# Optimization experiments

Measured on AMD Instinct MI355X. Metric: run time of the kernel, lower is better.

## Reference

```python
import jax, jax.numpy as jnp
import numpy as np

T, B, D, H, OUT = 128, 256, 512, 768, 60


def setup_inputs() -> dict:
    key = jax.random.key(0)
    ks = jax.random.split(key, 8)
    def xavier(k, shape):
        fan_out, fan_in = shape
        limit = np.sqrt(6.0 / (fan_in + fan_out))
        return jax.random.uniform(k, shape, jnp.float32, -limit, limit)
    inp = {
        "input_sample": jax.random.normal(ks[0], (T, B, D), jnp.float32),
        # PyTorch LSTMCell params: weight_ih (4H, D), weight_hh (4H, H), biases (4H,)
        "W_ih": xavier(ks[1], (4 * H, D)),
        "W_hh": xavier(ks[2], (4 * H, H)),
        "b_ih": jax.random.uniform(ks[3], (4 * H,), jnp.float32, -1 / np.sqrt(H), 1 / np.sqrt(H)),
        "b_hh": jax.random.uniform(ks[4], (4 * H,), jnp.float32, -1 / np.sqrt(H), 1 / np.sqrt(H)),
        "W_fc": xavier(ks[5], (OUT, H)),
        "b_fc": jnp.zeros((OUT,), jnp.float32),
    }
    return inp


def _lstm_head(input_sample, W_ih, W_hh, b_ih, b_hh, W_fc, b_fc):
    B_ = input_sample.shape[1]
    H_ = W_hh.shape[1]
    # Precompute input projections for all time steps in one GEMM: (T, B, 4H)
    x_proj = jnp.einsum("tbd,gd->tbg", input_sample, W_ih) + b_ih + b_hh

    def step(carry, xp_t):
        h, c = carry
        gates = xp_t + h @ W_hh.T  # (B, 4H)
        i, f, g, o = jnp.split(gates, 4, axis=-1)  # PyTorch gate order: i, f, g, o
        i = jax.nn.sigmoid(i)
        f = jax.nn.sigmoid(f)
        g = jnp.tanh(g)
        o = jax.nn.sigmoid(o)
        c_new = f * c + i * g
        h_new = o * jnp.tanh(c_new)
        return (h_new, c_new), None

    h0 = jnp.zeros((B_, H_), input_sample.dtype)
    c0 = jnp.zeros((B_, H_), input_sample.dtype)
    (h_T, _), _ = jax.lax.scan(step, (h0, c0), x_proj)
    return h_T @ W_fc.T + b_fc  # (B, OUT)


def reference(input_sample, W_ih, W_hh, b_ih, b_hh, W_fc, b_fc):
    return _lstm_head(input_sample, W_ih, W_hh, b_ih, b_hh, W_fc, b_fc)
```

## Files before the change

kernel.cpp:

```cpp
#include <hip/hip_runtime.h>
#include <stdint.h>

#define T_ 128
#define B_ 256
#define D_ 512
#define H_ 768
#define NG 3072
#define OUT_ 60

using bf16x8 = __attribute__((ext_vector_type(8))) __bf16;
using f32x4  = __attribute__((ext_vector_type(4))) float;
using u32x4  = __attribute__((ext_vector_type(4))) unsigned int;

#define OFF_XB   ((size_t)0)
#define OFF_WI   (OFF_XB + (size_t)T_*B_*D_*2)
#define OFF_WHPK (OFF_WI + (size_t)NG*D_*2)
#define OFF_H    (OFF_WHPK + (size_t)NG*H_*2)
#define OFF_HT   (OFF_H + (size_t)2*B_*H_*2)
#define OFF_BAR  (OFF_HT + (size_t)B_*H_*4)
#define OFF_XP   (OFF_BAR + 65536)
#define OFF_END  (OFF_XP + (size_t)T_*B_*NG*2)

__device__ __forceinline__ unsigned short f2bf(float f) {
  union { float f; unsigned u; } v; v.f = f;
  unsigned r = (v.u + 0x7fffu + ((v.u >> 16) & 1u)) >> 16;
  return (unsigned short)r;
}
__device__ __forceinline__ float sigf(float x) {
  return __builtin_amdgcn_rcpf(1.0f + __expf(-x));
}
__device__ __forceinline__ float tanhf_(float x) {
  return 2.0f * __builtin_amdgcn_rcpf(1.0f + __expf(-2.0f * x)) - 1.0f;
}
__device__ __forceinline__ void gload16(const void* g, void* l) {
  __builtin_amdgcn_global_load_lds(
      (const __attribute__((address_space(1))) unsigned int*)g,
      (__attribute__((address_space(3))) unsigned int*)l, 16, 0, 0);
}
template<int OFF, bool SC1>
__device__ __forceinline__ u32x4 ld16(const void* p) {
  u32x4 r;
  if constexpr (SC1)
    asm volatile("global_load_dwordx4 %0, %1, off offset:%c2 sc0 sc1"
                 : "=v"(r) : "v"(p), "i"(OFF) : "memory");
  else
    asm volatile("global_load_dwordx4 %0, %1, off offset:%c2 sc0"
                 : "=v"(r) : "v"(p), "i"(OFF) : "memory");
  return r;
}
__device__ __forceinline__ unsigned ld4coh(const unsigned* p) {
  unsigned r;
  asm volatile("global_load_dword %0, %1, off sc0 sc1\n\ts_waitcnt vmcnt(0)"
               : "=v"(r) : "v"(p) : "memory");
  return r;
}
template<bool SC1>
__device__ __forceinline__ void st2(ushort* p, unsigned v) {
  if constexpr (SC1)
    asm volatile("global_store_short %0, %1, off sc0 sc1" :: "v"(p), "v"(v) : "memory");
  else
    asm volatile("global_store_short %0, %1, off sc0" :: "v"(p), "v"(v) : "memory");
}
__device__ __forceinline__ void st4coh(unsigned* p, unsigned v) {
  asm volatile("global_store_dword %0, %1, off sc0 sc1" :: "v"(p), "v"(v) : "memory");
}

__global__ void prep_kernel(const float* __restrict__ x,
                            const float* __restrict__ wihf,
                            const float* __restrict__ whhf,
                            uint8_t* __restrict__ ws) {
  ushort* xb = (ushort*)(ws + OFF_XB);
  ushort* wi = (ushort*)(ws + OFF_WI);
  ushort* whpk = (ushort*)(ws + OFF_WHPK);
  unsigned* bar = (unsigned*)(ws + OFF_BAR);
  const size_t tid = (size_t)blockIdx.x * blockDim.x + threadIdx.x;
  const size_t nth = (size_t)gridDim.x * blockDim.x;

  for (size_t i = tid; i < (size_t)T_*B_*D_/4; i += nth) {
    float4 v = ((const float4*)x)[i];
    ushort4 o; o.x=f2bf(v.x); o.y=f2bf(v.y); o.z=f2bf(v.z); o.w=f2bf(v.w);
    ((ushort4*)xb)[i] = o;
  }
  for (size_t i = tid; i < (size_t)NG*D_/4; i += nth) {
    float4 v = ((const float4*)wihf)[i];
    ushort4 o; o.x=f2bf(v.x); o.y=f2bf(v.y); o.z=f2bf(v.z); o.w=f2bf(v.w);
    ((ushort4*)wi)[i] = o;
  }
  for (size_t c = tid; c < (size_t)294912; c += nth) {
    const unsigned L = (unsigned)c & 63u;
    const unsigned r1 = (unsigned)(c >> 6);
    const unsigned nt = r1 % 6u, r2 = r1 / 6u;
    const unsigned kf = r2 % 24u, s = r2 / 24u;
    const unsigned i = nt*16u + (L & 15u);
    const unsigned G = (i & 3u)*768u + s*24u + (i >> 2);
    const unsigned k0 = kf*32u + (L >> 4)*8u;
    const float4 v0 = *(const float4*)(whhf + (size_t)G*768u + k0);
    const float4 v1 = *(const float4*)(whhf + (size_t)G*768u + k0 + 4);
    ushort4 o0, o1;
    o0.x=f2bf(v0.x); o0.y=f2bf(v0.y); o0.z=f2bf(v0.z); o0.w=f2bf(v0.w);
    o1.x=f2bf(v1.x); o1.y=f2bf(v1.y); o1.z=f2bf(v1.z); o1.w=f2bf(v1.w);
    *(ushort4*)(whpk + c*8)     = o0;
    *(ushort4*)(whpk + c*8 + 4) = o1;
  }
  for (size_t i = tid; i < 16384; i += nth) bar[i] = 0u;
}

__global__ __launch_bounds__(256) void xproj_kernel(uint8_t* __restrict__ ws) {
  const ushort* __restrict__ xb = (const ushort*)(ws + OFF_XB);
  const ushort* __restrict__ wi = (const ushort*)(ws + OFF_WI);
  ushort* __restrict__ xp = (ushort*)(ws + OFF_XP);

  __shared__ ushort smA[128*64];
  __shared__ ushort smB[128*64];

  const int tid = threadIdx.x;
  const int lane = tid & 63;
  const int w = tid >> 6;
  const int bn = blockIdx.x % 24;
  const int bm = blockIdx.x / 24;
  const int m0 = bm * 128, n0 = bn * 128;
  const int mi = (w >> 1) * 64, ni = (w & 1) * 64;

  f32x4 acc[4][4] = {};

  for (int k0 = 0; k0 < D_; k0 += 64) {
    __syncthreads();
    #pragma unroll
    for (int i = 0; i < 4; ++i) {
      const int ig = w*4 + i;
      const int o  = ig*1024 + lane*16;
      const int row = o >> 7;
      const int colB = o & 127;
      const int scol = colB ^ ((row & 7) << 4);
      gload16((const uint8_t*)xb + ((size_t)(m0+row)*D_ + k0)*2 + scol,
              (uint8_t*)smA + ig*1024);
      gload16((const uint8_t*)wi + ((size_t)(n0+row)*D_ + k0)*2 + scol,
              (uint8_t*)smB + ig*1024);
    }
    __syncthreads();
    #pragma unroll
    for (int kk = 0; kk < 2; ++kk) {
      const int colB = kk*64 + (lane >> 4)*16;
      bf16x8 a[4], b[4];
      #pragma unroll
      for (int mt = 0; mt < 4; ++mt) {
        const int row = mi + mt*16 + (lane & 15);
        a[mt] = *(const bf16x8*)((const uint8_t*)smA + row*128 + (colB ^ ((row & 7) << 4)));
      }
      #pragma unroll
      for (int nt = 0; nt < 4; ++nt) {
        const int row = ni + nt*16 + (lane & 15);
        b[nt] = *(const bf16x8*)((const uint8_t*)smB + row*128 + (colB ^ ((row & 7) << 4)));
      }
      #pragma unroll
      for (int mt = 0; mt < 4; ++mt)
        #pragma unroll
        for (int nt = 0; nt < 4; ++nt)
          acc[mt][nt] = __builtin_amdgcn_mfma_f32_16x16x32_bf16(a[mt], b[nt], acc[mt][nt], 0, 0, 0);
    }
  }
  #pragma unroll
  for (int mt = 0; mt < 4; ++mt)
    #pragma unroll
    for (int nt = 0; nt < 4; ++nt) {
      const int r0 = m0 + mi + mt*16 + (lane >> 4)*4;
      const int c  = n0 + ni + nt*16 + (lane & 15);
      #pragma unroll
      for (int r = 0; r < 4; ++r)
        xp[(size_t)(r0 + r)*NG + c] = f2bf(acc[mt][nt][r]);
    }
}

template<bool SC1>
__device__ __forceinline__ void run_loop(uint8_t* ws, const ushort* whh_lds, float* gbuf,
                                         const float* bih, const float* bhh,
                                         int tid, int g, int s) {
  const int lane = tid & 63, w = tid >> 6, wq = w & 1, wm = w >> 1;
  const int l15 = lane & 15, hi = lane >> 4;
  ushort* hb = (ushort*)(ws + OFF_H);
  const ushort* xp = (const ushort*)(ws + OFF_XP);
  float* hT = (float*)(ws + OFF_HT);
  unsigned* bar = (unsigned*)(ws + OFF_BAR);
  float* gw = gbuf + w*816;

  float bias[3][4];
  #pragma unroll
  for (int j = 0; j < 3; ++j) {
    const int col = s*24 + wq*12 + hi + 4*j;
    #pragma unroll
    for (int q = 0; q < 4; ++q) bias[j][q] = bih[q*H_ + col] + bhh[q*H_ + col];
  }
  const unsigned* fp = bar + (size_t)(g*32 + ((lane < 32) ? lane : 31)) * 16;

  const ushort* xpb = xp + (size_t)(g*32 + wm*16 + l15)*NG + s*24 + wq*12 + hi;
  ushort xq[12];
  {
    const ushort* p = xpb;
    #pragma unroll
    for (int q = 0; q < 4; ++q)
      #pragma unroll
      for (int j = 0; j < 3; ++j)
        xq[q*3+j] = p[q*768 + 4*j];
  }

  float cc[3] = {0.f, 0.f, 0.f};

  #pragma unroll 1
  for (int t = 0; t < T_; ++t) {
    f32x4 acc[3] = {};
    if (t > 0) {
      if (w == 0) {
        while (1) {
          const unsigned v = ld4coh(fp);
          if (__all((int)(v >= (unsigned)t))) break;
          __builtin_amdgcn_s_sleep(1);
        }
      }
      __syncthreads();
      const ushort* hr = hb + ((size_t)(t & 1)*8 + g)*((size_t)32*H_)
                         + (size_t)(wm*16 + l15)*H_ + hi*8;
      u32x4 ah[24];
      #define LH(i) ah[i] = ld16<(i)*64, SC1>(hr)
      LH(0); LH(1); LH(2); LH(3); LH(4); LH(5); LH(6); LH(7);
      LH(8); LH(9); LH(10); LH(11); LH(12); LH(13); LH(14); LH(15);
      LH(16); LH(17); LH(18); LH(19); LH(20); LH(21); LH(22); LH(23);
      #undef LH
      asm volatile("s_waitcnt vmcnt(0)" ::: "memory");
      __builtin_amdgcn_sched_barrier(0);
      #pragma unroll
      for (int kf = 0; kf < 24; ++kf) {
        const bf16x8 a = *(const bf16x8*)&ah[kf];
        #pragma unroll
        for (int n = 0; n < 3; ++n) {
          const bf16x8 b = *(const bf16x8*)(whh_lds + (size_t)((kf*6 + wq*3 + n)*64 + lane)*8);
          acc[n] = __builtin_amdgcn_mfma_f32_16x16x32_bf16(a, b, acc[n], 0, 0, 0);
        }
      }
    }
    #pragma unroll
    for (int n = 0; n < 3; ++n)
      #pragma unroll
      for (int r = 0; r < 4; ++r)
        gw[(n*16 + l15)*17 + hi*4 + r] = acc[n][r];
    float hv[3];
    #pragma unroll
    for (int j = 0; j < 3; ++j) {
      const int cl = hi + 4*j;
      float gq[4];
      #pragma unroll
      for (int q = 0; q < 4; ++q) {
        union { unsigned u; float f; } xv; xv.u = ((unsigned)xq[q*3 + j]) << 16;
        gq[q] = gw[(cl*4+q)*17 + l15] + xv.f + bias[j][q];
      }
      const float iv = sigf(gq[0]);
      const float fv = sigf(gq[1]);
      const float gv = tanhf_(gq[2]);
      const float ov = sigf(gq[3]);
      const float cn = fv*cc[j] + iv*gv;
      cc[j] = cn;
      hv[j] = ov * tanhf_(cn);
    }
    const int rowl = wm*16 + l15;
    if (t == T_-1) {
      #pragma unroll
      for (int j = 0; j < 3; ++j) {
        const int col = s*24 + wq*12 + hi + 4*j;
        hT[(size_t)(g*32 + rowl)*H_ + col] = hv[j];
      }
      break;
    }
    ushort* hn = hb + ((size_t)((t+1) & 1)*8 + g)*((size_t)32*H_);
    #pragma unroll
    for (int j = 0; j < 3; ++j) {
      const int col = s*24 + wq*12 + hi + 4*j;
      st2<SC1>(hn + (size_t)rowl*H_ + col, (unsigned)f2bf(hv[j]));
    }
    asm volatile("s_waitcnt vmcnt(0)" ::: "memory");
    __syncthreads();
    if (tid == 0) st4coh(bar + (size_t)(g*32 + s)*16, (unsigned)(t + 1));
    {
      const ushort* p = xpb + (size_t)(t + 1)*B_*NG;
      #pragma unroll
      for (int q = 0; q < 4; ++q)
        #pragma unroll
        for (int j = 0; j < 3; ++j)
          xq[q*3+j] = p[q*768 + 4*j];
    }
  }
}

__global__ __launch_bounds__(256, 1) void lstm_kernel(uint8_t* __restrict__ ws,
                                                      const float* __restrict__ bih,
                                                      const float* __restrict__ bhh) {
  __shared__ ushort whh_lds[73728];
  __shared__ float gbuf[3264];
  const int tid = threadIdx.x, lane = tid & 63, w = tid >> 6;
  const int g = blockIdx.x & 7, s = blockIdx.x >> 3;
  unsigned* bar = (unsigned*)(ws + OFF_BAR);

  const uint8_t* wsrc = ws + OFF_WHPK + (size_t)s*9216*16;
  #pragma unroll
  for (int i = 0; i < 36; ++i) {
    const int cb = (w*36 + i)*64;
    gload16(wsrc + (size_t)(cb + lane)*16, (uint8_t*)whh_lds + (size_t)cb*16);
  }

  const unsigned xcd = __builtin_amdgcn_s_getreg((3 << 11) | 20) & 7u;
  if (tid == 0) {
    st4coh(bar + 4096 + blockIdx.x, xcd);
    asm volatile("s_waitcnt vmcnt(0)" ::: "memory");
    __hip_atomic_fetch_add(bar + 5120, 1u, __ATOMIC_RELAXED, __HIP_MEMORY_SCOPE_SYSTEM);
    while (__hip_atomic_load(bar + 5120, __ATOMIC_RELAXED, __HIP_MEMORY_SCOPE_SYSTEM) < 256u)
      __builtin_amdgcn_s_sleep(2);
  }
  __syncthreads();
  const int pl = (lane < 32) ? lane : 31;
  const unsigned oxcc = ld4coh(bar + 4096 + g + 8*pl);
  const bool local = __all((int)(oxcc == xcd));

  asm volatile("s_waitcnt vmcnt(0) lgkmcnt(0)" ::: "memory");
  __syncthreads();

  if (local) run_loop<false>(ws, whh_lds, gbuf, bih, bhh, tid, g, s);
  else       run_loop<true >(ws, whh_lds, gbuf, bih, bhh, tid, g, s);
}

__global__ __launch_bounds__(64) void fc_kernel(const uint8_t* __restrict__ ws,
                                                const float* __restrict__ wfc,
                                                const float* __restrict__ bfc,
                                                float* __restrict__ out) {
  const float* hT = (const float*)(ws + OFF_HT);
  const int b = blockIdx.x;
  const int lane = threadIdx.x;
  const float* hr = hT + (size_t)b*H_;
  float hv[12];
  #pragma unroll
  for (int i = 0; i < 12; ++i) hv[i] = hr[lane + i*64];
  for (int o = 0; o < OUT_; ++o) {
    const float* wr = wfc + (size_t)o*H_;
    float sum = 0.f;
    #pragma unroll
    for (int i = 0; i < 12; ++i) sum += hv[i] * wr[lane + i*64];
    #pragma unroll
    for (int off = 32; off; off >>= 1) sum += __shfl_xor(sum, off);
    if (lane == 0) out[(size_t)b*OUT_ + o] = sum + bfc[o];
  }
}

extern "C" void kernel_launch(void* const* d_in, const int* in_sizes, int n_in,
                              void* d_out, int out_size, void* d_ws, size_t ws_size,
                              hipStream_t stream) {
  const float* x   = (const float*)d_in[0];
  const float* wih = (const float*)d_in[1];
  const float* whh = (const float*)d_in[2];
  const float* bih = (const float*)d_in[3];
  const float* bhh = (const float*)d_in[4];
  const float* wfc = (const float*)d_in[5];
  const float* bfc = (const float*)d_in[6];
  uint8_t* ws = (uint8_t*)d_ws;
  float* out = (float*)d_out;

  prep_kernel<<<dim3(2048), dim3(256), 0, stream>>>(x, wih, whh, ws);
  xproj_kernel<<<dim3(256*24), dim3(256), 0, stream>>>(ws);
  lstm_kernel<<<dim3(256), dim3(256), 0, stream>>>(ws, bih, bhh);
  fc_kernel<<<dim3(256), dim3(64), 0, stream>>>(ws, wfc, bfc, out);
}
```

Before: 994.0 us.

## Replace persistent LSTM kernel with per-timestep kernel launches

```diff
diff --git a/kernel.cpp b/kernel.cpp
--- a/kernel.cpp
+++ b/kernel.cpp
@@ -17,8 +17,8 @@
 #define OFF_WHPK (OFF_WI + (size_t)NG*D_*2)
 #define OFF_H    (OFF_WHPK + (size_t)NG*H_*2)
 #define OFF_HT   (OFF_H + (size_t)2*B_*H_*2)
-#define OFF_BAR  (OFF_HT + (size_t)B_*H_*4)
-#define OFF_XP   (OFF_BAR + 65536)
+#define OFF_C    (OFF_HT + (size_t)B_*H_*4)
+#define OFF_XP   (OFF_C + (size_t)B_*H_*4)
 #define OFF_END  (OFF_XP + (size_t)T_*B_*NG*2)
 
 __device__ __forceinline__ unsigned short f2bf(float f) {
@@ -36,33 +36,6 @@
   __builtin_amdgcn_global_load_lds(
       (const __attribute__((address_space(1))) unsigned int*)g,
       (__attribute__((address_space(3))) unsigned int*)l, 16, 0, 0);
-}
-template<int OFF, bool SC1>
-__device__ __forceinline__ u32x4 ld16(const void* p) {
-  u32x4 r;
-  if constexpr (SC1)
-    asm volatile("global_load_dwordx4 %0, %1, off offset:%c2 sc0 sc1"
-                 : "=v"(r) : "v"(p), "i"(OFF) : "memory");
-  else
-    asm volatile("global_load_dwordx4 %0, %1, off offset:%c2 sc0"
-                 : "=v"(r) : "v"(p), "i"(OFF) : "memory");
-  return r;
-}
-__device__ __forceinline__ unsigned ld4coh(const unsigned* p) {
-  unsigned r;
-  asm volatile("global_load_dword %0, %1, off sc0 sc1\n\ts_waitcnt vmcnt(0)"
-               : "=v"(r) : "v"(p) : "memory");
-  return r;
-}
-template<bool SC1>
-__device__ __forceinline__ void st2(ushort* p, unsigned v) {
-  if constexpr (SC1)
-    asm volatile("global_store_short %0, %1, off sc0 sc1" :: "v"(p), "v"(v) : "memory");
-  else
-    asm volatile("global_store_short %0, %1, off sc0" :: "v"(p), "v"(v) : "memory");
-}
-__device__ __forceinline__ void st4coh(unsigned* p, unsigned v) {
-  asm volatile("global_store_dword %0, %1, off sc0 sc1" :: "v"(p), "v"(v) : "memory");
 }
 
 __global__ void prep_kernel(const float* __restrict__ x,
@@ -72,7 +45,8 @@
   ushort* xb = (ushort*)(ws + OFF_XB);
   ushort* wi = (ushort*)(ws + OFF_WI);
   ushort* whpk = (ushort*)(ws + OFF_WHPK);
-  unsigned* bar = (unsigned*)(ws + OFF_BAR);
+  unsigned* hb0 = (unsigned*)(ws + OFF_H);
+  float* cbuf = (float*)(ws + OFF_C);
   const size_t tid = (size_t)blockIdx.x * blockDim.x + threadIdx.x;
   const size_t nth = (size_t)gridDim.x * blockDim.x;
 
@@ -102,7 +76,8 @@
     *(ushort4*)(whpk + c*8)     = o0;
     *(ushort4*)(whpk + c*8 + 4) = o1;
   }
-  for (size_t i = tid; i < 16384; i += nth) bar[i] = 0u;
+  for (size_t i = tid; i < (size_t)B_*H_/2; i += nth) hb0[i] = 0u;
+  for (size_t i = tid; i < (size_t)B_*H_; i += nth) cbuf[i] = 0.f;
 }
 
 __global__ __launch_bounds__(256) void xproj_kernel(uint8_t* __restrict__ ws) {
@@ -171,16 +146,20 @@
     }
 }
 
-template<bool SC1>
-__device__ __forceinline__ void run_loop(uint8_t* ws, const ushort* whh_lds, float* gbuf,
-                                         const float* bih, const float* bhh,
-                                         int tid, int g, int s) {
-  const int lane = tid & 63, w = tid >> 6, wq = w & 1, wm = w >> 1;
+__global__ __launch_bounds__(256) void step_kernel(uint8_t* __restrict__ ws,
+                                                   const float* __restrict__ bih,
+                                                   const float* __restrict__ bhh,
+                                                   int t) {
+  __shared__ float gbuf[3264];
+  __shared__ ushort hstage[768];
+  const int tid = threadIdx.x, lane = tid & 63, w = tid >> 6, wq = w & 1, wm = w >> 1;
   const int l15 = lane & 15, hi = lane >> 4;
-  ushort* hb = (ushort*)(ws + OFF_H);
-  const ushort* xp = (const ushort*)(ws + OFF_XP);
-  float* hT = (float*)(ws + OFF_HT);
-  unsigned* bar = (unsigned*)(ws + OFF_BAR);
+  const int gp = blockIdx.x & 3, s = blockIdx.x >> 2;
+  const ushort* __restrict__ whpk = (const ushort*)(ws + OFF_WHPK);
+  ushort* __restrict__ hb = (ushort*)(ws + OFF_H);
+  float* __restrict__ hT = (float*)(ws + OFF_HT);
+  float* __restrict__ cbuf = (float*)(ws + OFF_C);
+  const ushort* __restrict__ xp = (const ushort*)(ws + OFF_XP);
   float* gw = gbuf + w*816;
 
   float bias[3][4];
@@ -190,51 +169,33 @@
     #pragma unroll
     for (int q = 0; q < 4; ++q) bias[j][q] = bih[q*H_ + col] + bhh[q*H_ + col];
   }
-  const unsigned* fp = bar + (size_t)(g*32 + ((lane < 32) ? lane : 31)) * 16;
-
-  const ushort* xpb = xp + (size_t)(g*32 + wm*16 + l15)*NG + s*24 + wq*12 + hi;
-  ushort xq[12];
-  {
-    const ushort* p = xpb;
+  const ushort* wb = whpk + (size_t)s*9216*8;
+
+  #pragma unroll 1
+  for (int gg = 0; gg < 2; ++gg) {
+    const int g = gp*2 + gg;
+    const ushort* hr = hb + ((size_t)(t & 1)*8 + g)*((size_t)32*H_)
+                       + (size_t)(wm*16 + l15)*H_ + hi*8;
+    u32x4 ah[24];
+    #pragma unroll
+    for (int kf = 0; kf < 24; ++kf)
+      ah[kf] = *(const u32x4*)((const uint8_t*)hr + kf*64);
+    const ushort* xpb = xp + ((size_t)t*B_ + g*32 + wm*16 + l15)*NG + s*24 + wq*12 + hi;
+    ushort xq[12];
     #pragma unroll
     for (int q = 0; q < 4; ++q)
       #pragma unroll
       for (int j = 0; j < 3; ++j)
-        xq[q*3+j] = p[q*768 + 4*j];
-  }
-
-  float cc[3] = {0.f, 0.f, 0.f};
-
-  #pragma unroll 1
-  for (int t = 0; t < T_; ++t) {
+        xq[q*3+j] = xpb[q*H_ + 4*j];
+
     f32x4 acc[3] = {};
-    if (t > 0) {
-      if (w == 0) {
-        while (1) {
-          const unsigned v = ld4coh(fp);
-          if (__all((int)(v >= (unsigned)t))) break;
-          __builtin_amdgcn_s_sleep(1);
-        }
-      }
-      __syncthreads();
-      const ushort* hr = hb + ((size_t)(t & 1)*8 + g)*((size_t)32*H_)
-                         + (size_t)(wm*16 + l15)*H_ + hi*8;
-      u32x4 ah[24];
-      #define LH(i) ah[i] = ld16<(i)*64, SC1>(hr)
-      LH(0); LH(1); LH(2); LH(3); LH(4); LH(5); LH(6); LH(7);
-      LH(8); LH(9); LH(10); LH(11); LH(12); LH(13); LH(14); LH(15);
-      LH(16); LH(17); LH(18); LH(19); LH(20); LH(21); LH(22); LH(23);
-      #undef LH
-      asm volatile("s_waitcnt vmcnt(0)" ::: "memory");
-      __builtin_amdgcn_sched_barrier(0);
-      #pragma unroll
-      for (int kf = 0; kf < 24; ++kf) {
-        const bf16x8 a = *(const bf16x8*)&ah[kf];
-        #pragma unroll
-        for (int n = 0; n < 3; ++n) {
-          const bf16x8 b = *(const bf16x8*)(whh_lds + (size_t)((kf*6 + wq*3 + n)*64 + lane)*8);
-          acc[n] = __builtin_amdgcn_mfma_f32_16x16x32_bf16(a, b, acc[n], 0, 0, 0);
-        }
+    #pragma unroll
+    for (int kf = 0; kf < 24; ++kf) {
+      const bf16x8 a = *(const bf16x8*)&ah[kf];
+      #pragma unroll
+      for (int n = 0; n < 3; ++n) {
+        const bf16x8 b = *(const bf16x8*)(wb + (size_t)((kf*6 + wq*3 + n)*64 + lane)*8);
+        acc[n] = __builtin_amdgcn_mfma_f32_16x16x32_bf16(a, b, acc[n], 0, 0, 0);
       }
     }
     #pragma unroll
@@ -242,6 +203,9 @@
       #pragma unroll
       for (int r = 0; r < 4; ++r)
         gw[(n*16 + l15)*17 + hi*4 + r] = acc[n][r];
+
+    const int rowl = wm*16 + l15;
+    float* cp = cbuf + (size_t)(g*32 + rowl)*H_ + s*24 + wq*12 + hi;
     float hv[3];
     #pragma unroll
     for (int j = 0; j < 3; ++j) {
@@ -256,73 +220,30 @@
       const float fv = sigf(gq[1]);
       const float gv = tanhf_(gq[2]);
       const float ov = sigf(gq[3]);
-      const float cn = fv*cc[j] + iv*gv;
-      cc[j] = cn;
+      const float cn = fv*cp[4*j] + iv*gv;
+      cp[4*j] = cn;
       hv[j] = ov * tanhf_(cn);
     }
-    const int rowl = wm*16 + l15;
     if (t == T_-1) {
       #pragma unroll
       for (int j = 0; j < 3; ++j) {
         const int col = s*24 + wq*12 + hi + 4*j;
         hT[(size_t)(g*32 + rowl)*H_ + col] = hv[j];
       }
-      break;
-    }
-    ushort* hn = hb + ((size_t)((t+1) & 1)*8 + g)*((size_t)32*H_);
-    #pragma unroll
-    for (int j = 0; j < 3; ++j) {
-      const int col = s*24 + wq*12 + hi + 4*j;
-      st2<SC1>(hn + (size_t)rowl*H_ + col, (unsigned)f2bf(hv[j]));
-    }
-    asm volatile("s_waitcnt vmcnt(0)" ::: "memory");
-    __syncthreads();
-    if (tid == 0) st4coh(bar + (size_t)(g*32 + s)*16, (unsigned)(t + 1));
-    {
-      const ushort* p = xpb + (size_t)(t + 1)*B_*NG;
-      #pragma unroll
-      for (int q = 0; q < 4; ++q)
-        #pragma unroll
-        for (int j = 0; j < 3; ++j)
-          xq[q*3+j] = p[q*768 + 4*j];
-    }
-  }
-}
-
-__global__ __launch_bounds__(256, 1) void lstm_kernel(uint8_t* __restrict__ ws,
-                                                      const float* __restrict__ bih,
-                                                      const float* __restrict__ bhh) {
-  __shared__ ushort whh_lds[73728];
-  __shared__ float gbuf[3264];
-  const int tid = threadIdx.x, lane = tid & 63, w = tid >> 6;
-  const int g = blockIdx.x & 7, s = blockIdx.x >> 3;
-  unsigned* bar = (unsigned*)(ws + OFF_BAR);
-
-  const uint8_t* wsrc = ws + OFF_WHPK + (size_t)s*9216*16;
-  #pragma unroll
-  for (int i = 0; i < 36; ++i) {
-    const int cb = (w*36 + i)*64;
-    gload16(wsrc + (size_t)(cb + lane)*16, (uint8_t*)whh_lds + (size_t)cb*16);
-  }
-
-  const unsigned xcd = __builtin_amdgcn_s_getreg((3 << 11) | 20) & 7u;
-  if (tid == 0) {
-    st4coh(bar + 4096 + blockIdx.x, xcd);
-    asm volatile("s_waitcnt vmcnt(0)" ::: "memory");
-    __hip_atomic_fetch_add(bar + 5120, 1u, __ATOMIC_RELAXED, __HIP_MEMORY_SCOPE_SYSTEM);
-    while (__hip_atomic_load(bar + 5120, __ATOMIC_RELAXED, __HIP_MEMORY_SCOPE_SYSTEM) < 256u)
-      __builtin_amdgcn_s_sleep(2);
-  }
-  __syncthreads();
-  const int pl = (lane < 32) ? lane : 31;
-  const unsigned oxcc = ld4coh(bar + 4096 + g + 8*pl);
-  const bool local = __all((int)(oxcc == xcd));
-
-  asm volatile("s_waitcnt vmcnt(0) lgkmcnt(0)" ::: "memory");
-  __syncthreads();
-
-  if (local) run_loop<false>(ws, whh_lds, gbuf, bih, bhh, tid, g, s);
-  else       run_loop<true >(ws, whh_lds, gbuf, bih, bhh, tid, g, s);
+    } else {
+      #pragma unroll
+      for (int j = 0; j < 3; ++j)
+        hstage[rowl*24 + wq*12 + hi + 4*j] = f2bf(hv[j]);
+      __syncthreads();
+      ushort* hn = hb + ((size_t)((t+1) & 1)*8 + g)*((size_t)32*H_);
+      if (tid < 96) {
+        const int row = tid / 3, part = tid % 3;
+        const u32x4 v = *(const u32x4*)((const uint8_t*)hstage + row*48 + part*16);
+        *(u32x4*)(hn + (size_t)row*H_ + s*24 + part*8) = v;
+      }
+      __syncthreads();
+    }
+  }
 }
 
 __global__ __launch_bounds__(64) void fc_kernel(const uint8_t* __restrict__ ws,
@@ -362,6 +283,7 @@
 
   prep_kernel<<<dim3(2048), dim3(256), 0, stream>>>(x, wih, whh, ws);
   xproj_kernel<<<dim3(256*24), dim3(256), 0, stream>>>(ws);
-  lstm_kernel<<<dim3(256), dim3(256), 0, stream>>>(ws, bih, bhh);
+  for (int t = 0; t < T_; ++t)
+    step_kernel<<<dim3(128), dim3(256), 0, stream>>>(ws, bih, bhh, t);
   fc_kernel<<<dim3(256), dim3(64), 0, stream>>>(ws, wfc, bfc, out);
 }
```

After: 2.234 ms (median of 2 runs). 2.25x slower.

## Pipeline per-chunk flag waits with h loads and coalesce h stores via LDS

Applied to the files above, without the earlier changes.

```diff
diff --git a/kernel.cpp b/kernel.cpp
--- a/kernel.cpp
+++ b/kernel.cpp
@@ -55,11 +55,11 @@
   return r;
 }
 template<bool SC1>
-__device__ __forceinline__ void st2(ushort* p, unsigned v) {
+__device__ __forceinline__ void st16g(void* p, u32x4 v) {
   if constexpr (SC1)
-    asm volatile("global_store_short %0, %1, off sc0 sc1" :: "v"(p), "v"(v) : "memory");
+    asm volatile("global_store_dwordx4 %0, %1, off sc0 sc1" :: "v"(p), "v"(v) : "memory");
   else
-    asm volatile("global_store_short %0, %1, off sc0" :: "v"(p), "v"(v) : "memory");
+    asm volatile("global_store_dwordx4 %0, %1, off sc0" :: "v"(p), "v"(v) : "memory");
 }
 __device__ __forceinline__ void st4coh(unsigned* p, unsigned v) {
   asm volatile("global_store_dword %0, %1, off sc0 sc1" :: "v"(p), "v"(v) : "memory");
@@ -102,7 +102,7 @@
     *(ushort4*)(whpk + c*8)     = o0;
     *(ushort4*)(whpk + c*8 + 4) = o1;
   }
-  for (size_t i = tid; i < 16384; i += nth) bar[i] = 0u;
+  for (size_t i = tid; i < 16384; i += nth) st4coh(&bar[i], 0u);
 }
 
 __global__ __launch_bounds__(256) void xproj_kernel(uint8_t* __restrict__ ws) {
@@ -173,6 +173,7 @@
 
 template<bool SC1>
 __device__ __forceinline__ void run_loop(uint8_t* ws, const ushort* whh_lds, float* gbuf,
+                                         ushort* hstage,
                                          const float* bih, const float* bhh,
                                          int tid, int g, int s) {
   const int lane = tid & 63, w = tid >> 6, wq = w & 1, wm = w >> 1;
@@ -190,7 +191,6 @@
     #pragma unroll
     for (int q = 0; q < 4; ++q) bias[j][q] = bih[q*H_ + col] + bhh[q*H_ + col];
   }
-  const unsigned* fp = bar + (size_t)(g*32 + ((lane < 32) ? lane : 31)) * 16;
 
   const ushort* xpb = xp + (size_t)(g*32 + wm*16 + l15)*NG + s*24 + wq*12 + hi;
   ushort xq[12];
@@ -209,31 +209,31 @@
   for (int t = 0; t < T_; ++t) {
     f32x4 acc[3] = {};
     if (t > 0) {
-      if (w == 0) {
+      const uint8_t* hr = (const uint8_t*)(hb + ((size_t)(t & 1)*8 + g)*((size_t)32*H_)
+                          + (size_t)(wm*16 + l15)*H_ + hi*8);
+      #pragma unroll 1
+      for (int ch = 0; ch < 8; ++ch) {
+        const unsigned* fp = bar + (size_t)(g*32 + ch*4 + (lane & 3)) * 16;
         while (1) {
           const unsigned v = ld4coh(fp);
           if (__all((int)(v >= (unsigned)t))) break;
           __builtin_amdgcn_s_sleep(1);
         }
-      }
-      __syncthreads();
-      const ushort* hr = hb + ((size_t)(t & 1)*8 + g)*((size_t)32*H_)
-                         + (size_t)(wm*16 + l15)*H_ + hi*8;
-      u32x4 ah[24];
-      #define LH(i) ah[i] = ld16<(i)*64, SC1>(hr)
-      LH(0); LH(1); LH(2); LH(3); LH(4); LH(5); LH(6); LH(7);
-      LH(8); LH(9); LH(10); LH(11); LH(12); LH(13); LH(14); LH(15);
-      LH(16); LH(17); LH(18); LH(19); LH(20); LH(21); LH(22); LH(23);
-      #undef LH
-      asm volatile("s_waitcnt vmcnt(0)" ::: "memory");
-      __builtin_amdgcn_sched_barrier(0);
-      #pragma unroll
-      for (int kf = 0; kf < 24; ++kf) {
-        const bf16x8 a = *(const bf16x8*)&ah[kf];
+        u32x4 a0 = ld16<  0, SC1>(hr + ch*192);
+        u32x4 a1 = ld16< 64, SC1>(hr + ch*192);
+        u32x4 a2 = ld16<128, SC1>(hr + ch*192);
+        asm volatile("s_waitcnt vmcnt(0)" ::: "memory");
+        __builtin_amdgcn_sched_barrier(0);
         #pragma unroll
-        for (int n = 0; n < 3; ++n) {
-          const bf16x8 b = *(const bf16x8*)(whh_lds + (size_t)((kf*6 + wq*3 + n)*64 + lane)*8);
-          acc[n] = __builtin_amdgcn_mfma_f32_16x16x32_bf16(a, b, acc[n], 0, 0, 0);
+        for (int kk = 0; kk < 3; ++kk) {
+          const int kf = ch*3 + kk;
+          const bf16x8 a = (kk == 0) ? *(const bf16x8*)&a0
+                         : (kk == 1) ? *(const bf16x8*)&a1 : *(const bf16x8*)&a2;
+          #pragma unroll
+          for (int n = 0; n < 3; ++n) {
+            const bf16x8 b = *(const bf16x8*)(whh_lds + (size_t)((kf*6 + wq*3 + n)*64 + lane)*8);
+            acc[n] = __builtin_amdgcn_mfma_f32_16x16x32_bf16(a, b, acc[n], 0, 0, 0);
+          }
         }
       }
     }
@@ -269,11 +269,15 @@
       }
       break;
     }
+    #pragma unroll
+    for (int j = 0; j < 3; ++j)
+      hstage[rowl*24 + wq*12 + hi + 4*j] = f2bf(hv[j]);
+    __syncthreads();
     ushort* hn = hb + ((size_t)((t+1) & 1)*8 + g)*((size_t)32*H_);
-    #pragma unroll
-    for (int j = 0; j < 3; ++j) {
-      const int col = s*24 + wq*12 + hi + 4*j;
-      st2<SC1>(hn + (size_t)rowl*H_ + col, (unsigned)f2bf(hv[j]));
+    if (tid < 96) {
+      const int row = tid / 3, part = tid % 3;
+      const u32x4 v = *(const u32x4*)((const uint8_t*)hstage + row*48 + part*16);
+      st16g<SC1>(hn + (size_t)row*H_ + s*24 + part*8, v);
     }
     asm volatile("s_waitcnt vmcnt(0)" ::: "memory");
     __syncthreads();
@@ -294,6 +298,7 @@
                                                       const float* __restrict__ bhh) {
   __shared__ ushort whh_lds[73728];
   __shared__ float gbuf[3264];
+  __shared__ ushort hstage[768];
   const int tid = threadIdx.x, lane = tid & 63, w = tid >> 6;
   const int g = blockIdx.x & 7, s = blockIdx.x >> 3;
   unsigned* bar = (unsigned*)(ws + OFF_BAR);
@@ -321,8 +326,8 @@
   asm volatile("s_waitcnt vmcnt(0) lgkmcnt(0)" ::: "memory");
   __syncthreads();
 
-  if (local) run_loop<false>(ws, whh_lds, gbuf, bih, bhh, tid, g, s);
-  else       run_loop<true >(ws, whh_lds, gbuf, bih, bhh, tid, g, s);
+  if (local) run_loop<false>(ws, whh_lds, gbuf, hstage, bih, bhh, tid, g, s);
+  else       run_loop<true >(ws, whh_lds, gbuf, hstage, bih, bhh, tid, g, s);
 }
 
 __global__ __launch_bounds__(64) void fc_kernel(const uint8_t* __restrict__ ws,
```

New measurement: 1.133 ms. +14.0%, slower.
